# Performance work log

Measured on AMD Instinct MI355X. Metric: run time of the kernel, lower is better.

## Reference

```python
import jax, jax.numpy as jnp
import numpy as np
from jax.scipy.special import gammainc

ALPH = 0.8  # significance level (default arg in original forward)


def _median_width(X, iu, ju):
    # pairwise squared distances; original takes median of strictly-positive
    # strict-upper-triangle entries (tril subtracted) -> median over triu(k=1)
    G = jnp.sum(X * X, axis=1)                    # [n]
    D = G[:, None] + G[None, :] - 2.0 * (X @ X.T)  # [n, n]
    du = D[iu, ju]                                 # strict upper triangle, static size
    return jnp.sqrt(0.5 * jnp.median(du))


def _rbf(X, width):
    G = jnp.sum(X * X, axis=1)
    D = G[:, None] + G[None, :] - 2.0 * (X @ X.T)
    return jnp.exp(-D / (2.0 * width ** 2))


def _center(K):
    # H K H with H = I - 11^T/n  ==  K - rowmean - colmean + totalmean
    cm = jnp.mean(K, axis=0, keepdims=True)   # mean over rows  -> [1, n]
    rm = jnp.mean(K, axis=1, keepdims=True)   # mean over cols  -> [n, 1]
    tm = jnp.mean(K)
    return K - cm - rm + tm


def _gamma_ppf(a, p):
    # invert regularized lower incomplete gamma via fixed-iteration bisection
    hi0 = a + 10.0 * jnp.sqrt(a) + 100.0
    def body(i, lohi):
        lo, hi = lohi
        mid = 0.5 * (lo + hi)
        below = gammainc(a, mid) < p
        return (jnp.where(below, mid, lo), jnp.where(below, hi, mid))
    lo, hi = jax.lax.fori_loop(0, 100, body, (jnp.zeros_like(a), hi0))
    return 0.5 * (lo + hi)


def setup_inputs() -> dict:
    key = jax.random.key(0)
    k1, k2 = jax.random.split(key)
    X = jax.random.normal(k1, (4096, 64), dtype=jnp.float32)
    Y = jax.random.normal(k2, (4096, 64), dtype=jnp.float32)
    return {"X": X, "Y": Y}


def reference(X, Y):
    n = X.shape[0]
    iu, ju = np.triu_indices(n, k=1)  # static index set

    width_x = _median_width(X, iu, ju)
    width_y = _median_width(Y, iu, ju)

    K = _rbf(X, width_x)
    L = _rbf(Y, width_y)

    Kc = _center(K)
    Lc = _center(L)

    testStat = jnp.sum(Kc.T * Lc) / n

    V = (Kc * Lc / 6.0) ** 2
    varHSIC = (jnp.sum(V) - jnp.trace(V)) / n / (n - 1)
    varHSIC = varHSIC * 72.0 * (n - 4) * (n - 5) / n / (n - 1) / (n - 2) / (n - 3)

    # zero-diagonal kernels for mean estimate
    K0sum = jnp.sum(K) - jnp.trace(K)
    L0sum = jnp.sum(L) - jnp.trace(L)
    muX = K0sum / n / (n - 1)
    muY = L0sum / n / (n - 1)
    mHSIC = (1.0 + muX * muY - muX - muY) / n

    al = mHSIC ** 2 / varHSIC
    bet = varHSIC * n / mHSIC
    thresh = bet * _gamma_ppf(al, jnp.float32(1.0 - ALPH))
    return (testStat, thresh)
```

## Files before the change

### kernel.cpp

```cpp
#include <hip/hip_runtime.h>

typedef unsigned int u32;
typedef unsigned short u16;
typedef __attribute__((ext_vector_type(8))) short bf16x8;
typedef __attribute__((ext_vector_type(4))) float f32x4;

#define NPTS 4096
#define DIM  64
#define NB   32
#define NBLK 528
#define WLO16 0x4140u
#define NWBIN 832
#define RSTR 836


__device__ __forceinline__ void bmap(int b, int& by, int& bx){
  by = 0;
  while (b >= NB - by){ b -= NB - by; by++; }
  bx = by + b;
}

__device__ __forceinline__ u16 f2bf(float x){
  u32 u = __float_as_uint(x);
  return (u16)((u + 0x7fffu + ((u>>16)&1u)) >> 16);
}

__global__ __launch_bounds__(256) void convert_k(const float* __restrict__ X, const float* __restrict__ Y,
                                                 u16* __restrict__ Xbf, float* __restrict__ Gall,
                                                 u32* __restrict__ histsum, double* __restrict__ rowK,
                                                 double* __restrict__ rowL, double* __restrict__ sums){
  int t = blockIdx.x*256 + threadIdx.x;
  int rid = t >> 1, hf = t & 1;
  int z = rid >> 12, row = rid & 4095;
  const float* src = (z ? Y : X) + (size_t)row*DIM + hf*32;
  u16* base = Xbf + ((size_t)z*32768 + (size_t)(row>>4)*128 + (row&15))*8;
  float g = 0.f;
#pragma unroll
  for (int f=0; f<4; f++){
    float4 f0 = *(const float4*)(src + f*8);
    float4 f1 = *(const float4*)(src + f*8 + 4);
    g = fmaf(f0.x,f0.x,g); g = fmaf(f0.y,f0.y,g); g = fmaf(f0.z,f0.z,g); g = fmaf(f0.w,f0.w,g);
    g = fmaf(f1.x,f1.x,g); g = fmaf(f1.y,f1.y,g); g = fmaf(f1.z,f1.z,g); g = fmaf(f1.w,f1.w,g);
    ushort4 h0, h1;
    h0.x=f2bf(f0.x); h0.y=f2bf(f0.y); h0.z=f2bf(f0.z); h0.w=f2bf(f0.w);
    h1.x=f2bf(f1.x); h1.y=f2bf(f1.y); h1.z=f2bf(f1.z); h1.w=f2bf(f1.w);
    u16* dst = base + (size_t)(hf*4 + f)*16*8;
    *(ushort4*)dst = h0;
    *(ushort4*)(dst+4) = h1;
  }
  g += __shfl_xor(g, 1, 64);
  if (hf==0) Gall[rid] = g;
  if (t < NPTS){ rowK[t] = 0.0; rowL[t] = 0.0; }
  if (t < 2*RSTR) histsum[t] = 0u;
  if (t < 2) sums[t] = 0.0;
}

__global__ __launch_bounds__(256,2) void hist_k(const u16* __restrict__ Xbf, const float* __restrict__ Gall,
                                                u32* __restrict__ histsum){
  __shared__ u32 lh[RSTR];
  int z = blockIdx.y, tid = threadIdx.x;
  int by,bx; bmap(blockIdx.x, by, bx);
  bool isdiag = (by==bx);
  u32 wgt = isdiag ? 1u : 2u;
  int w=tid>>6, lane=tid&63, q=lane>>4, nl=lane&15;
  for (int t=tid;t<RSTR;t+=256) lh[t]=0;
  __syncthreads();
  const bf16x8* Xb = (const bf16x8*)Xbf + (size_t)z*32768;
  const float* Gz = Gall + z*NPTS;
  int rt0 = w, rt1 = 4 + w;
  int ag0 = by*8 + rt0, ag1 = by*8 + rt1;
  bf16x8 a0f0 = Xb[ag0*128 + q*16 + nl];
  bf16x8 a0f1 = Xb[ag0*128 + (4+q)*16 + nl];
  bf16x8 a1f0 = Xb[ag1*128 + q*16 + nl];
  bf16x8 a1f1 = Xb[ag1*128 + (4+q)*16 + nl];
  float ga0 = Gz[ag0*16 + nl], ga1 = Gz[ag1*16 + nl];
  float g0m[4], g1m[4];
#pragma unroll
  for (int r=0;r<4;r++){ g0m[r] = __shfl(ga0, q*4+r, 64); g1m[r] = __shfl(ga1, q*4+r, 64); }
#pragma unroll
  for (int tb=0;tb<8;tb++){
    int jg = bx*8 + tb;
    bf16x8 bf0 = Xb[jg*128 + q*16 + nl];
    bf16x8 bf1 = Xb[jg*128 + (4+q)*16 + nl];
    f32x4 acc0 = (f32x4)0.0f, acc1 = (f32x4)0.0f;
    acc0 = __builtin_amdgcn_mfma_f32_16x16x32_bf16(a0f0, bf0, acc0, 0,0,0);
    acc0 = __builtin_amdgcn_mfma_f32_16x16x32_bf16(a0f1, bf1, acc0, 0,0,0);
    acc1 = __builtin_amdgcn_mfma_f32_16x16x32_bf16(a1f0, bf0, acc1, 0,0,0);
    acc1 = __builtin_amdgcn_mfma_f32_16x16x32_bf16(a1f1, bf1, acc1, 0,0,0);
    int j = jg*16 + nl;
    float gb = Gz[j];
#pragma unroll
    for (int r=0;r<4;r++){
      float d0 = (g0m[r] + gb) - 2.0f*acc0[r];
      float d1 = (g1m[r] + gb) - 2.0f*acc1[r];
      if (isdiag){
        if (ag0*16 + q*4 + r == j) d0 = 0.f;
        if (ag1*16 + q*4 + r == j) d1 = 0.f;
      }
      u32 t0 = __float_as_uint(d0) >> 16;
      u32 b0 = (t0 < WLO16) ? 0u : (t0 >= WLO16+NWBIN) ? (u32)(NWBIN+1) : (t0 - WLO16 + 1u);
      atomicAdd(&lh[b0], wgt);
      u32 t1 = __float_as_uint(d1) >> 16;
      u32 b1 = (t1 < WLO16) ? 0u : (t1 >= WLO16+NWBIN) ? (u32)(NWBIN+1) : (t1 - WLO16 + 1u);
      atomicAdd(&lh[b1], wgt);
    }
  }
  __syncthreads();
  u32* dst = histsum + (size_t)z*RSTR;
  for (int t=tid;t<RSTR;t+=256){
    u32 v = lh[t];
    if (v) atomicAdd(&dst[t], v);
  }
}

__global__ __launch_bounds__(256) void scan16i(const u32* __restrict__ histsum,
                                               float* __restrict__ scal,
                                               u32 kf1, u32 kf2){
  int z = blockIdx.x;
  int tid = threadIdx.x;
  __shared__ u32 wsum[4];
  __shared__ double svals[2];
  u32 c4[4] = {0,0,0,0};
  if (tid < 209){
    const u32* base = histsum + (size_t)z*RSTR + 4*tid;
    int lim = RSTR - 4*tid;
    c4[0] = base[0];
    if (lim>1) c4[1] = base[1];
    if (lim>2) c4[2] = base[2];
    if (lim>3) c4[3] = base[3];
  }
  u32 s = c4[0]+c4[1]+c4[2]+c4[3];
  int lane = tid & 63, wv = tid >> 6;
  u32 pre = s;
#pragma unroll
  for (int off=1; off<64; off<<=1){
    u32 t2 = __shfl_up(pre, off, 64);
    if (lane >= off) pre += t2;
  }
  if (lane==63) wsum[wv] = pre;
  __syncthreads();
  u32 base2 = 0;
  for (int k=0;k<wv;k++) base2 += wsum[k];
  u32 incl = base2 + pre, excl = incl - s;
  u32 ks[2] = {kf1,kf2};
#pragma unroll
  for (int w2=0; w2<2; w2++){
    if (ks[w2] >= excl && ks[w2] < incl){
      u32 acc = excl;
#pragma unroll
      for (int j=0;j<4;j++){
        if (ks[w2] < acc + c4[j]){
          int b = tid*4 + j;
          double lo, hi;
          if (b==0){ lo=12.0; hi=12.0; }
          else if (b>=NWBIN+1){ lo=1024.0; hi=1024.0; }
          else {
            u32 t16 = WLO16 + (u32)b - 1u;
            lo = (double)__uint_as_float(t16<<16);
            hi = (double)__uint_as_float((t16+1u)<<16);
          }
          double frac = ((double)(ks[w2]-acc) + 0.5)/(double)c4[j];
          svals[w2] = lo + (hi-lo)*frac;
          break;
        }
        acc += c4[j];
      }
    }
  }
  __syncthreads();
  if (tid==0){
    float med = (float)(0.5*(svals[0]+svals[1]));
    float wd = sqrtf(0.5f*med);
    scal[z] = 2.0f*wd*wd;
  }
}

__global__ __launch_bounds__(256,2) void rowsum_k(const u16* __restrict__ Xbf, const float* __restrict__ Gall,
                                                  const float* __restrict__ scal,
                                                  double* __restrict__ rowK, double* __restrict__ rowL,
                                                  double* __restrict__ sums){
  __shared__ double rowacc[128];
  __shared__ double colLDS[4][128];
  __shared__ double tred[2];
  int z = blockIdx.y, tid = threadIdx.x;
  int by,bx; bmap(blockIdx.x, by, bx);
  bool isdiag = (by==bx);
  int w=tid>>6, lane=tid&63, q=lane>>4, nl=lane&15;
  const bf16x8* Xb = (const bf16x8*)Xbf + (size_t)z*32768;
  const float* Gz = Gall + z*NPTS;
  float negi = -1.0f/scal[z];
  int rt0 = w, rt1 = 4 + w;
  int ag0 = by*8 + rt0, ag1 = by*8 + rt1;
  bf16x8 a0f0 = Xb[ag0*128 + q*16 + nl];
  bf16x8 a0f1 = Xb[ag0*128 + (4+q)*16 + nl];
  bf16x8 a1f0 = Xb[ag1*128 + q*16 + nl];
  bf16x8 a1f1 = Xb[ag1*128 + (4+q)*16 + nl];
  float ga0 = Gz[ag0*16 + nl], ga1 = Gz[ag1*16 + nl];
  float g0m[4], g1m[4];
#pragma unroll
  for (int r=0;r<4;r++){ g0m[r] = __shfl(ga0, q*4+r, 64); g1m[r] = __shfl(ga1, q*4+r, 64); }
  double rs0[4] = {0,0,0,0}, rs1[4] = {0,0,0,0};
#pragma unroll
  for (int tb=0;tb<8;tb++){
    int jg = bx*8 + tb;
    bf16x8 bf0 = Xb[jg*128 + q*16 + nl];
    bf16x8 bf1 = Xb[jg*128 + (4+q)*16 + nl];
    f32x4 acc0 = (f32x4)0.0f, acc1 = (f32x4)0.0f;
    acc0 = __builtin_amdgcn_mfma_f32_16x16x32_bf16(a0f0, bf0, acc0, 0,0,0);
    acc0 = __builtin_amdgcn_mfma_f32_16x16x32_bf16(a0f1, bf1, acc0, 0,0,0);
    acc1 = __builtin_amdgcn_mfma_f32_16x16x32_bf16(a1f0, bf0, acc1, 0,0,0);
    acc1 = __builtin_amdgcn_mfma_f32_16x16x32_bf16(a1f1, bf1, acc1, 0,0,0);
    int j = jg*16 + nl;
    float gb = Gz[j];
    double cs = 0.0;
#pragma unroll
    for (int r=0;r<4;r++){
      float d0 = (g0m[r] + gb) - 2.0f*acc0[r];
      float d1 = (g1m[r] + gb) - 2.0f*acc1[r];
      if (isdiag){
        if (ag0*16 + q*4 + r == j) d0 = 0.f;
        if (ag1*16 + q*4 + r == j) d1 = 0.f;
      }
      double e0 = (double)expf(d0*negi);
      double e1 = (double)expf(d1*negi);
      rs0[r] += e0; rs1[r] += e1;
      cs += e0 + e1;
    }
    cs += __shfl_xor(cs, 16, 64);
    cs += __shfl_xor(cs, 32, 64);
    if (q==0) colLDS[w][tb*16 + nl] = cs;
  }
#pragma unroll
  for (int r=0;r<4;r++){
    double v0 = rs0[r], v1 = rs1[r];
    v0 += __shfl_xor(v0,1,64); v0 += __shfl_xor(v0,2,64);
    v0 += __shfl_xor(v0,4,64); v0 += __shfl_xor(v0,8,64);
    v1 += __shfl_xor(v1,1,64); v1 += __shfl_xor(v1,2,64);
    v1 += __shfl_xor(v1,4,64); v1 += __shfl_xor(v1,8,64);
    rs0[r] = v0; rs1[r] = v1;
  }
  if (nl==0){
#pragma unroll
    for (int r=0;r<4;r++){
      rowacc[rt0*16 + q*4 + r] = rs0[r];
      rowacc[rt1*16 + q*4 + r] = rs1[r];
    }
  }
  __syncthreads();
  double tot = 0.0;
  if (tid < 128){
    double rv = rowacc[tid];
    double cv = colLDS[0][tid] + colLDS[1][tid] + colLDS[2][tid] + colLDS[3][tid];
    double* rowG = z ? rowL : rowK;
    atomicAdd(&rowG[by*128 + tid], rv);
    if (!isdiag) atomicAdd(&rowG[bx*128 + tid], cv);
    tot = rv + (isdiag ? 0.0 : cv);
  }
#pragma unroll
  for (int s2=1;s2<64;s2<<=1) tot += __shfl_xor(tot, s2, 64);
  if (lane==0 && w<2) tred[w] = tot;
  __syncthreads();
  if (tid==0) atomicAdd(&sums[z], tred[0] + tred[1]);
}

__global__ __launch_bounds__(256,2) void final_k(const u16* __restrict__ Xbf, const float* __restrict__ Gall,
                                                 const float* __restrict__ scal,
                                                 const double* __restrict__ rowK,
                                                 const double* __restrict__ rowL,
                                                 const double* __restrict__ sums,
                                                 double* __restrict__ partials){
  int tid = threadIdx.x;
  int b = blockIdx.x >> 1, half = blockIdx.x & 1;
  int by,bx; bmap(b,by,bx);
  bool isdiag = (by==bx);
  int w=tid>>6, lane=tid&63, q=lane>>4, nl=lane&15;
  const bf16x8* Xb = (const bf16x8*)Xbf;
  const bf16x8* Yb = Xb + 32768;
  const float* Gx = Gall;
  const float* Gy = Gall + NPTS;
  const double inv_n = 1.0/(double)NPTS;
  double tmK = sums[0]*(inv_n*inv_n), tmL = sums[1]*(inv_n*inv_n);
  float negx = -1.0f/scal[0], negy = -1.0f/scal[1];
  double wgt = isdiag ? 1.0 : 2.0;
  double S1=0, S2=0, trV=0;
  int rt = half*4 + w;
  int ag = by*8 + rt;
  bf16x8 axf0 = Xb[ag*128 + q*16 + nl];
  bf16x8 axf1 = Xb[ag*128 + (4+q)*16 + nl];
  bf16x8 ayf0 = Yb[ag*128 + q*16 + nl];
  bf16x8 ayf1 = Yb[ag*128 + (4+q)*16 + nl];
  int rowA = ag*16 + nl;
  float gaX = Gx[rowA], gaY = Gy[rowA];
  float gXm[4], gYm[4];
#pragma unroll
  for (int r=0;r<4;r++){ gXm[r] = __shfl(gaX, q*4+r, 64); gYm[r] = __shfl(gaY, q*4+r, 64); }
  double rmKi[4], rmLi[4];
#pragma unroll
  for (int r=0;r<4;r++){
    int i = ag*16 + q*4 + r;
    rmKi[r] = rowK[i]*inv_n; rmLi[r] = rowL[i]*inv_n;
  }
#pragma unroll
  for (int tb=0;tb<8;tb++){
    int jg = bx*8 + tb;
    f32x4 accX = (f32x4)0.0f, accY = (f32x4)0.0f;
    accX = __builtin_amdgcn_mfma_f32_16x16x32_bf16(axf0, Xb[jg*128 + q*16 + nl],     accX, 0,0,0);
    accX = __builtin_amdgcn_mfma_f32_16x16x32_bf16(axf1, Xb[jg*128 + (4+q)*16 + nl], accX, 0,0,0);
    accY = __builtin_amdgcn_mfma_f32_16x16x32_bf16(ayf0, Yb[jg*128 + q*16 + nl],     accY, 0,0,0);
    accY = __builtin_amdgcn_mfma_f32_16x16x32_bf16(ayf1, Yb[jg*128 + (4+q)*16 + nl], accY, 0,0,0);
    int j = jg*16 + nl;
    float gbX = Gx[j], gbY = Gy[j];
    double cmK = rowK[j]*inv_n - tmK;
    double cmL = rowL[j]*inv_n - tmL;
#pragma unroll
    for (int r=0;r<4;r++){
      int i = ag*16 + q*4 + r;
      float dx = (gXm[r] + gbX) - 2.0f*accX[r];
      float dy = (gYm[r] + gbY) - 2.0f*accY[r];
      bool dg = isdiag && i==j;
      if (dg){ dx = 0.f; dy = 0.f; }
      float kx = expf(dx*negx);
      float lv = expf(dy*negy);
      double kc = ((double)kx - rmKi[r]) - cmK;
      double lc = ((double)lv - rmLi[r]) - cmL;
      double prod = kc*lc;
      S1 += wgt*prod;
      double vv = (prod*prod)*(1.0/36.0);
      S2 += wgt*vv;
      if (dg) trV += vv;
    }
  }
  __shared__ double red[4][3];
  double vals[3]={S1,S2,trV};
  int wv = tid >> 6;
#pragma unroll
  for (int v=0;v<3;v++){
    double x = vals[v];
#pragma unroll
    for (int s2=1;s2<64;s2<<=1) x += __shfl_xor(x, s2, 64);
    if (lane==0) red[wv][v]=x;
  }
  __syncthreads();
  if (tid < 3)
    partials[(size_t)blockIdx.x*4 + tid] = red[0][tid]+red[1][tid]+red[2][tid]+red[3][tid];
}

__device__ double gammainc_wave(double a, double x, double lga, int lane){
  double C = 1.0/a;
  double psum = 0.0;
  for (int b=0;b<8192;b++){
    double k = (double)(b*64 + lane + 1);
    double rr = x/(a+k);
    double pp = rr;
#pragma unroll
    for (int s=1;s<64;s<<=1){
      double t = __shfl_up(pp, s, 64);
      if (lane >= s) pp *= t;
    }
    double c = C*pp;
    psum += c;
    double clast = __shfl(c, 63, 64);
    double rlast = __shfl(rr, 63, 64);
    C = clast;
    if (rlast < 1.0 && clast*rlast/(1.0-rlast) < 1e-17) break;
  }
#pragma unroll
  for (int s=1;s<64;s<<=1) psum += __shfl_xor(psum, s, 64);
  double total = 1.0/a + psum;
  return exp(-x + a*log(x) - lga) * total;
}

__global__ __launch_bounds__(256) void finalize_k(const double* __restrict__ partials,
                                                  const double* __restrict__ sums,
                                                  float* __restrict__ out)
{
  __shared__ double red[3][4];
  __shared__ double tot[4];
  int tid = threadIdx.x;
  double v0=0,v1=0,v2=0;
  for (int i=tid; i<2*NBLK; i+=256){
    const double* p = partials + (size_t)i*4;
    v0+=p[0]; v1+=p[1]; v2+=p[2];
  }
  double vals[3]={v0,v1,v2};
  int lane = tid & 63, wv = tid >> 6;
#pragma unroll
  for (int v=0;v<3;v++){
    double x = vals[v];
#pragma unroll
    for (int s2=1;s2<64;s2<<=1) x += __shfl_xor(x, s2, 64);
    if (lane==0) red[v][wv]=x;
  }
  __syncthreads();
  if (tid==0){
#pragma unroll
    for (int v=0;v<3;v++) tot[v] = red[v][0]+red[v][1]+red[v][2]+red[v][3];
  }
  __syncthreads();
  if (tid >= 64) return;

  const double n = (double)NPTS;
  double totK=sums[0], totL=sums[1];
  double S1=tot[0], S2=tot[1], trV=tot[2];
  double testStat = S1/n;
  double varHSIC = (S2 - trV)/n/(n-1.0);
  varHSIC = varHSIC*72.0*(n-4.0)*(n-5.0)/n/(n-1.0)/(n-2.0)/(n-3.0);
  double muX = (totK-n)/n/(n-1.0);
  double muY = (totL-n)/n/(n-1.0);
  double mHSIC = (1.0 + muX*muY - muX - muY)/n;
  double al = mHSIC*mHSIC/varHSIC;
  double bet = varHSIC*n/mHSIC;
  double p = (double)((float)(1.0-0.8));
  double lga = lgamma(al);
  double lo = 0.0, hi = al + 10.0*sqrt(al) + 100.0;
  const double zp = -0.8416212335729142957;
  double t = 1.0 - 1.0/(9.0*al) + zp/(3.0*sqrt(al));
  double x = al*t*t*t;
  if (!(x > 0.0) || !(x < hi)) x = 0.5*hi;
  for (int it=0; it<2; ++it){
    double P = gammainc_wave(al, x, lga, lane);
    double diff = P - p;
    if (diff < 0.0) lo = x; else hi = x;
    if (fabs(diff) < 1e-12) break;
    double pdf = exp(-x + (al-1.0)*log(x) - lga);
    double nx = x - diff/pdf;
    if (!(nx > lo) || !(nx < hi)) nx = 0.5*(lo+hi);
    x = nx;
  }
  if (lane==0){
    out[0]=(float)testStat;
    out[1]=(float)(bet*x);
  }
}

extern "C" void kernel_launch(void* const* d_in, const int* in_sizes, int n_in,
                              void* d_out, int out_size, void* d_ws, size_t ws_size,
                              hipStream_t stream) {
  const float* X = (const float*)d_in[0];
  const float* Y = (const float*)d_in[1];
  float* out = (float*)d_out;
  char* ws = (char*)d_ws;

  double* sums     = (double*)ws;
  float*  scal     = (float*)(ws + 128);
  u32*    histsum  = (u32*)(ws + 256);
  double* rowK     = (double*)(ws + 8192);
  double* rowL     = (double*)(ws + 40960);
  float*  Gall     = (float*)(ws + 73728);
  double* partials = (double*)(ws + 106496);
  u16*    Xbf      = (u16*)(ws + (4u<<20));
  size_t need = (size_t)(4u<<20) + (size_t)2*NPTS*DIM*2;

  if (ws_size < need) return;

  const u32 KF1 = 4096u + 2u*4193279u;
  const u32 KF2 = 4096u + 2u*4193280u;

  convert_k<<<64,256,0,stream>>>(X, Y, Xbf, Gall, histsum, rowK, rowL, sums);
  hist_k<<<dim3(NBLK,2),256,0,stream>>>(Xbf, Gall, histsum);
  scan16i<<<2,256,0,stream>>>(histsum, scal, KF1, KF2);
  rowsum_k<<<dim3(NBLK,2),256,0,stream>>>(Xbf, Gall, scal, rowK, rowL, sums);
  final_k<<<2*NBLK,256,0,stream>>>(Xbf, Gall, scal, rowK, rowL, sums, partials);
  finalize_k<<<1,256,0,stream>>>(partials, sums, out);
}
```

Baseline: 146.9 us.

## Fuse median scan into rowsum, last-block finalize, and privatize histograms

Every rowsum block now redundantly runs the histogram prefix scan to find the median width, so the separate scan kernel launch goes away. The final reduction and gamma-quantile solve move into final_k, where a global atomic counter elects the last block to do them, removing the finalize kernel launch. The per-block LDS histogram is split into four lane-indexed copies to cut atomic contention, and global double sums are spread over slots to reduce same-address atomics. In exchange, every rowsum block repeats the scan work, and the last final_k block carries the serial gamma computation.

Result: slower. 153.6 us (+4.6%).

```diff
diff --git a/kernel.cpp b/kernel.cpp
--- a/kernel.cpp
+++ b/kernel.cpp
@@ -12,6 +12,8 @@
 #define WLO16 0x4140u
 #define NWBIN 832
 #define RSTR 836
+#define KF1C 8390654u
+#define KF2C 8390656u
 
 
 __device__ __forceinline__ void bmap(int b, int& by, int& bx){
@@ -28,12 +30,13 @@
 __global__ __launch_bounds__(256) void convert_k(const float* __restrict__ X, const float* __restrict__ Y,
                                                  u16* __restrict__ Xbf, float* __restrict__ Gall,
                                                  u32* __restrict__ histsum, double* __restrict__ rowK,
-                                                 double* __restrict__ rowL, double* __restrict__ sums){
+                                                 double* __restrict__ rowL, double* __restrict__ sumsS,
+                                                 double* __restrict__ slotbuf, u32* __restrict__ ctr){
   int t = blockIdx.x*256 + threadIdx.x;
   int rid = t >> 1, hf = t & 1;
   int z = rid >> 12, row = rid & 4095;
   const float* src = (z ? Y : X) + (size_t)row*DIM + hf*32;
-  u16* base = Xbf + ((size_t)z*32768 + (size_t)(row>>4)*128 + (row&15))*8;
+  u16* basep = Xbf + ((size_t)z*32768 + (size_t)(row>>4)*128 + (row&15))*8;
   float g = 0.f;
 #pragma unroll
   for (int f=0; f<4; f++){
@@ -44,7 +47,7 @@
     ushort4 h0, h1;
     h0.x=f2bf(f0.x); h0.y=f2bf(f0.y); h0.z=f2bf(f0.z); h0.w=f2bf(f0.w);
     h1.x=f2bf(f1.x); h1.y=f2bf(f1.y); h1.z=f2bf(f1.z); h1.w=f2bf(f1.w);
-    u16* dst = base + (size_t)(hf*4 + f)*16*8;
+    u16* dst = basep + (size_t)(hf*4 + f)*16*8;
     *(ushort4*)dst = h0;
     *(ushort4*)(dst+4) = h1;
   }
@@ -52,23 +55,25 @@
   if (hf==0) Gall[rid] = g;
   if (t < NPTS){ rowK[t] = 0.0; rowL[t] = 0.0; }
   if (t < 2*RSTR) histsum[t] = 0u;
-  if (t < 2) sums[t] = 0.0;
+  if (t < 64) slotbuf[t] = 0.0;
+  if (t < 16) sumsS[t] = 0.0;
+  if (t == 0) *ctr = 0u;
 }
 
 __global__ __launch_bounds__(256,2) void hist_k(const u16* __restrict__ Xbf, const float* __restrict__ Gall,
                                                 u32* __restrict__ histsum){
-  __shared__ u32 lh[RSTR];
+  __shared__ u32 lh[4][RSTR];
   int z = blockIdx.y, tid = threadIdx.x;
   int by,bx; bmap(blockIdx.x, by, bx);
   bool isdiag = (by==bx);
   u32 wgt = isdiag ? 1u : 2u;
   int w=tid>>6, lane=tid&63, q=lane>>4, nl=lane&15;
-  for (int t=tid;t<RSTR;t+=256) lh[t]=0;
+  int cp = lane & 3;
+  for (int t=tid;t<4*RSTR;t+=256) ((u32*)lh)[t]=0;
   __syncthreads();
   const bf16x8* Xb = (const bf16x8*)Xbf + (size_t)z*32768;
   const float* Gz = Gall + z*NPTS;
-  int rt0 = w, rt1 = 4 + w;
-  int ag0 = by*8 + rt0, ag1 = by*8 + rt1;
+  int ag0 = by*8 + w, ag1 = by*8 + 4 + w;
   bf16x8 a0f0 = Xb[ag0*128 + q*16 + nl];
   bf16x8 a0f1 = Xb[ag0*128 + (4+q)*16 + nl];
   bf16x8 a1f0 = Xb[ag1*128 + q*16 + nl];
@@ -98,99 +103,97 @@
         if (ag1*16 + q*4 + r == j) d1 = 0.f;
       }
       u32 t0 = __float_as_uint(d0) >> 16;
-      u32 b0 = (t0 < WLO16) ? 0u : (t0 >= WLO16+NWBIN) ? (u32)(NWBIN+1) : (t0 - WLO16 + 1u);
-      atomicAdd(&lh[b0], wgt);
+      u32 bin0 = (t0 < WLO16) ? 0u : (t0 >= WLO16+NWBIN) ? (u32)(NWBIN+1) : (t0 - WLO16 + 1u);
+      atomicAdd(&lh[cp][bin0], wgt);
       u32 t1 = __float_as_uint(d1) >> 16;
-      u32 b1 = (t1 < WLO16) ? 0u : (t1 >= WLO16+NWBIN) ? (u32)(NWBIN+1) : (t1 - WLO16 + 1u);
-      atomicAdd(&lh[b1], wgt);
+      u32 bin1 = (t1 < WLO16) ? 0u : (t1 >= WLO16+NWBIN) ? (u32)(NWBIN+1) : (t1 - WLO16 + 1u);
+      atomicAdd(&lh[cp][bin1], wgt);
     }
   }
   __syncthreads();
   u32* dst = histsum + (size_t)z*RSTR;
   for (int t=tid;t<RSTR;t+=256){
-    u32 v = lh[t];
+    u32 v = lh[0][t] + lh[1][t] + lh[2][t] + lh[3][t];
     if (v) atomicAdd(&dst[t], v);
   }
 }
 
-__global__ __launch_bounds__(256) void scan16i(const u32* __restrict__ histsum,
-                                               float* __restrict__ scal,
-                                               u32 kf1, u32 kf2){
-  int z = blockIdx.x;
-  int tid = threadIdx.x;
-  __shared__ u32 wsum[4];
-  __shared__ double svals[2];
-  u32 c4[4] = {0,0,0,0};
-  if (tid < 209){
-    const u32* base = histsum + (size_t)z*RSTR + 4*tid;
-    int lim = RSTR - 4*tid;
-    c4[0] = base[0];
-    if (lim>1) c4[1] = base[1];
-    if (lim>2) c4[2] = base[2];
-    if (lim>3) c4[3] = base[3];
-  }
-  u32 s = c4[0]+c4[1]+c4[2]+c4[3];
-  int lane = tid & 63, wv = tid >> 6;
-  u32 pre = s;
-#pragma unroll
-  for (int off=1; off<64; off<<=1){
-    u32 t2 = __shfl_up(pre, off, 64);
-    if (lane >= off) pre += t2;
-  }
-  if (lane==63) wsum[wv] = pre;
-  __syncthreads();
-  u32 base2 = 0;
-  for (int k=0;k<wv;k++) base2 += wsum[k];
-  u32 incl = base2 + pre, excl = incl - s;
-  u32 ks[2] = {kf1,kf2};
-#pragma unroll
-  for (int w2=0; w2<2; w2++){
-    if (ks[w2] >= excl && ks[w2] < incl){
-      u32 acc = excl;
-#pragma unroll
-      for (int j=0;j<4;j++){
-        if (ks[w2] < acc + c4[j]){
-          int b = tid*4 + j;
-          double lo, hi;
-          if (b==0){ lo=12.0; hi=12.0; }
-          else if (b>=NWBIN+1){ lo=1024.0; hi=1024.0; }
-          else {
-            u32 t16 = WLO16 + (u32)b - 1u;
-            lo = (double)__uint_as_float(t16<<16);
-            hi = (double)__uint_as_float((t16+1u)<<16);
+__global__ __launch_bounds__(256,2) void rowsum_k(const u16* __restrict__ Xbf, const float* __restrict__ Gall,
+                                                  const u32* __restrict__ histsum, float* __restrict__ scal,
+                                                  double* __restrict__ rowK, double* __restrict__ rowL,
+                                                  double* __restrict__ sumsS){
+  __shared__ union {
+    struct { u32 wsum[4]; double svals[2]; float scal_sh; } sc;
+    struct { double rowacc[128]; double colLDS[4][128]; double tred[2]; } rs;
+  } sh;
+  int z = blockIdx.y, tid = threadIdx.x;
+  int w=tid>>6, lane=tid&63, q=lane>>4, nl=lane&15;
+
+  {
+    u32 c4[4] = {0,0,0,0};
+    if (tid < 209){
+      const u32* base = histsum + (size_t)z*RSTR + 4*tid;
+      int lim = RSTR - 4*tid;
+      c4[0] = base[0];
+      if (lim>1) c4[1] = base[1];
+      if (lim>2) c4[2] = base[2];
+      if (lim>3) c4[3] = base[3];
+    }
+    u32 s = c4[0]+c4[1]+c4[2]+c4[3];
+    u32 pre = s;
+#pragma unroll
+    for (int off=1; off<64; off<<=1){
+      u32 t2 = __shfl_up(pre, off, 64);
+      if (lane >= off) pre += t2;
+    }
+    if (lane==63) sh.sc.wsum[w] = pre;
+    __syncthreads();
+    u32 base2 = 0;
+    for (int k=0;k<w;k++) base2 += sh.sc.wsum[k];
+    u32 incl = base2 + pre, excl = incl - s;
+    u32 ks[2] = {KF1C,KF2C};
+#pragma unroll
+    for (int w2=0; w2<2; w2++){
+      if (ks[w2] >= excl && ks[w2] < incl){
+        u32 acc = excl;
+#pragma unroll
+        for (int j=0;j<4;j++){
+          if (ks[w2] < acc + c4[j]){
+            int b = tid*4 + j;
+            double lo, hi;
+            if (b==0){ lo=12.0; hi=12.0; }
+            else if (b>=NWBIN+1){ lo=1024.0; hi=1024.0; }
+            else {
+              u32 t16 = WLO16 + (u32)b - 1u;
+              lo = (double)__uint_as_float(t16<<16);
+              hi = (double)__uint_as_float((t16+1u)<<16);
+            }
+            double frac = ((double)(ks[w2]-acc) + 0.5)/(double)c4[j];
+            sh.sc.svals[w2] = lo + (hi-lo)*frac;
+            break;
           }
-          double frac = ((double)(ks[w2]-acc) + 0.5)/(double)c4[j];
-          svals[w2] = lo + (hi-lo)*frac;
-          break;
+          acc += c4[j];
         }
-        acc += c4[j];
       }
     }
-  }
-  __syncthreads();
-  if (tid==0){
-    float med = (float)(0.5*(svals[0]+svals[1]));
-    float wd = sqrtf(0.5f*med);
-    scal[z] = 2.0f*wd*wd;
-  }
-}
-
-__global__ __launch_bounds__(256,2) void rowsum_k(const u16* __restrict__ Xbf, const float* __restrict__ Gall,
-                                                  const float* __restrict__ scal,
-                                                  double* __restrict__ rowK, double* __restrict__ rowL,
-                                                  double* __restrict__ sums){
-  __shared__ double rowacc[128];
-  __shared__ double colLDS[4][128];
-  __shared__ double tred[2];
-  int z = blockIdx.y, tid = threadIdx.x;
+    __syncthreads();
+    if (tid==0){
+      float med = (float)(0.5*(sh.sc.svals[0]+sh.sc.svals[1]));
+      float wd = sqrtf(0.5f*med);
+      float sc2 = 2.0f*wd*wd;
+      sh.sc.scal_sh = sc2;
+      if (blockIdx.x==0) scal[z] = sc2;
+    }
+    __syncthreads();
+  }
+  float negi = -1.0f / sh.sc.scal_sh;
+  __syncthreads();
+
   int by,bx; bmap(blockIdx.x, by, bx);
   bool isdiag = (by==bx);
-  int w=tid>>6, lane=tid&63, q=lane>>4, nl=lane&15;
   const bf16x8* Xb = (const bf16x8*)Xbf + (size_t)z*32768;
   const float* Gz = Gall + z*NPTS;
-  float negi = -1.0f/scal[z];
-  int rt0 = w, rt1 = 4 + w;
-  int ag0 = by*8 + rt0, ag1 = by*8 + rt1;
+  int ag0 = by*8 + w, ag1 = by*8 + 4 + w;
   bf16x8 a0f0 = Xb[ag0*128 + q*16 + nl];
   bf16x8 a0f1 = Xb[ag0*128 + (4+q)*16 + nl];
   bf16x8 a1f0 = Xb[ag1*128 + q*16 + nl];
@@ -228,7 +231,7 @@
     }
     cs += __shfl_xor(cs, 16, 64);
     cs += __shfl_xor(cs, 32, 64);
-    if (q==0) colLDS[w][tb*16 + nl] = cs;
+    if (q==0) sh.rs.colLDS[w][tb*16 + nl] = cs;
   }
 #pragma unroll
   for (int r=0;r<4;r++){
@@ -242,15 +245,15 @@
   if (nl==0){
 #pragma unroll
     for (int r=0;r<4;r++){
-      rowacc[rt0*16 + q*4 + r] = rs0[r];
-      rowacc[rt1*16 + q*4 + r] = rs1[r];
+      sh.rs.rowacc[w*16 + q*4 + r]     = rs0[r];
+      sh.rs.rowacc[(4+w)*16 + q*4 + r] = rs1[r];
     }
   }
   __syncthreads();
   double tot = 0.0;
   if (tid < 128){
-    double rv = rowacc[tid];
-    double cv = colLDS[0][tid] + colLDS[1][tid] + colLDS[2][tid] + colLDS[3][tid];
+    double rv = sh.rs.rowacc[tid];
+    double cv = sh.rs.colLDS[0][tid] + sh.rs.colLDS[1][tid] + sh.rs.colLDS[2][tid] + sh.rs.colLDS[3][tid];
     double* rowG = z ? rowL : rowK;
     atomicAdd(&rowG[by*128 + tid], rv);
     if (!isdiag) atomicAdd(&rowG[bx*128 + tid], cv);
@@ -258,17 +261,45 @@
   }
 #pragma unroll
   for (int s2=1;s2<64;s2<<=1) tot += __shfl_xor(tot, s2, 64);
-  if (lane==0 && w<2) tred[w] = tot;
-  __syncthreads();
-  if (tid==0) atomicAdd(&sums[z], tred[0] + tred[1]);
+  if (lane==0 && w<2) sh.rs.tred[w] = tot;
+  __syncthreads();
+  if (tid==0) atomicAdd(&sumsS[z*8 + (blockIdx.x & 7)], sh.rs.tred[0] + sh.rs.tred[1]);
+}
+
+__device__ double gammainc_wave(double a, double x, double lga, int lane){
+  double C = 1.0/a;
+  double psum = 0.0;
+  for (int b=0;b<8192;b++){
+    double k = (double)(b*64 + lane + 1);
+    double rr = x/(a+k);
+    double pp = rr;
+#pragma unroll
+    for (int s=1;s<64;s<<=1){
+      double t = __shfl_up(pp, s, 64);
+      if (lane >= s) pp *= t;
+    }
+    double c = C*pp;
+    psum += c;
+    double clast = __shfl(c, 63, 64);
+    double rlast = __shfl(rr, 63, 64);
+    C = clast;
+    if (rlast < 1.0 && clast*rlast/(1.0-rlast) < 1e-17) break;
+  }
+#pragma unroll
+  for (int s=1;s<64;s<<=1) psum += __shfl_xor(psum, s, 64);
+  double total = 1.0/a + psum;
+  return exp(-x + a*log(x) - lga) * total;
 }
 
 __global__ __launch_bounds__(256,2) void final_k(const u16* __restrict__ Xbf, const float* __restrict__ Gall,
                                                  const float* __restrict__ scal,
                                                  const double* __restrict__ rowK,
                                                  const double* __restrict__ rowL,
-                                                 const double* __restrict__ sums,
-                                                 double* __restrict__ partials){
+                                                 const double* __restrict__ sumsS,
+                                                 double* __restrict__ slotbuf, u32* __restrict__ ctr,
+                                                 float* __restrict__ out){
+  __shared__ double red[4][3];
+  __shared__ int lastFlag;
   int tid = threadIdx.x;
   int b = blockIdx.x >> 1, half = blockIdx.x & 1;
   int by,bx; bmap(b,by,bx);
@@ -279,12 +310,14 @@
   const float* Gx = Gall;
   const float* Gy = Gall + NPTS;
   const double inv_n = 1.0/(double)NPTS;
-  double tmK = sums[0]*(inv_n*inv_n), tmL = sums[1]*(inv_n*inv_n);
+  double sK=0.0, sL=0.0;
+#pragma unroll
+  for (int k2=0;k2<8;k2++){ sK += sumsS[k2]; sL += sumsS[8+k2]; }
+  double tmK = sK*(inv_n*inv_n), tmL = sL*(inv_n*inv_n);
   float negx = -1.0f/scal[0], negy = -1.0f/scal[1];
   double wgt = isdiag ? 1.0 : 2.0;
   double S1=0, S2=0, trV=0;
-  int rt = half*4 + w;
-  int ag = by*8 + rt;
+  int ag = by*8 + half*4 + w;
   bf16x8 axf0 = Xb[ag*128 + q*16 + nl];
   bf16x8 axf1 = Xb[ag*128 + (4+q)*16 + nl];
   bf16x8 ayf0 = Yb[ag*128 + q*16 + nl];
@@ -330,83 +363,49 @@
       if (dg) trV += vv;
     }
   }
-  __shared__ double red[4][3];
   double vals[3]={S1,S2,trV};
-  int wv = tid >> 6;
 #pragma unroll
   for (int v=0;v<3;v++){
     double x = vals[v];
 #pragma unroll
     for (int s2=1;s2<64;s2<<=1) x += __shfl_xor(x, s2, 64);
-    if (lane==0) red[wv][v]=x;
-  }
-  __syncthreads();
-  if (tid < 3)
-    partials[(size_t)blockIdx.x*4 + tid] = red[0][tid]+red[1][tid]+red[2][tid]+red[3][tid];
-}
-
-__device__ double gammainc_wave(double a, double x, double lga, int lane){
-  double C = 1.0/a;
-  double psum = 0.0;
-  for (int b=0;b<8192;b++){
-    double k = (double)(b*64 + lane + 1);
-    double rr = x/(a+k);
-    double pp = rr;
-#pragma unroll
-    for (int s=1;s<64;s<<=1){
-      double t = __shfl_up(pp, s, 64);
-      if (lane >= s) pp *= t;
-    }
-    double c = C*pp;
-    psum += c;
-    double clast = __shfl(c, 63, 64);
-    double rlast = __shfl(rr, 63, 64);
-    C = clast;
-    if (rlast < 1.0 && clast*rlast/(1.0-rlast) < 1e-17) break;
-  }
-#pragma unroll
-  for (int s=1;s<64;s<<=1) psum += __shfl_xor(psum, s, 64);
-  double total = 1.0/a + psum;
-  return exp(-x + a*log(x) - lga) * total;
-}
-
-__global__ __launch_bounds__(256) void finalize_k(const double* __restrict__ partials,
-                                                  const double* __restrict__ sums,
-                                                  float* __restrict__ out)
-{
-  __shared__ double red[3][4];
-  __shared__ double tot[4];
-  int tid = threadIdx.x;
-  double v0=0,v1=0,v2=0;
-  for (int i=tid; i<2*NBLK; i+=256){
-    const double* p = partials + (size_t)i*4;
-    v0+=p[0]; v1+=p[1]; v2+=p[2];
-  }
-  double vals[3]={v0,v1,v2};
-  int lane = tid & 63, wv = tid >> 6;
-#pragma unroll
-  for (int v=0;v<3;v++){
-    double x = vals[v];
-#pragma unroll
-    for (int s2=1;s2<64;s2<<=1) x += __shfl_xor(x, s2, 64);
-    if (lane==0) red[v][wv]=x;
+    if (lane==0) red[w][v]=x;
+  }
+  __syncthreads();
+  if (tid < 3){
+    double val = red[0][tid]+red[1][tid]+red[2][tid]+red[3][tid];
+    atomicAdd(&slotbuf[(size_t)(blockIdx.x & 15)*4 + tid], val);
   }
   __syncthreads();
   if (tid==0){
-#pragma unroll
-    for (int v=0;v<3;v++) tot[v] = red[v][0]+red[v][1]+red[v][2]+red[v][3];
-  }
-  __syncthreads();
+    __threadfence();
+    u32 old = atomicAdd(ctr, 1u);
+    lastFlag = (old == (u32)(2*NBLK - 1)) ? 1 : 0;
+  }
+  __syncthreads();
+  if (!lastFlag) return;
+
   if (tid >= 64) return;
-
+  double t0=0.0, t1=0.0, t2=0.0;
+  if (lane < 16){
+    double* sp = slotbuf + (size_t)lane*4;
+    t0 = atomicAdd(&sp[0], 0.0);
+    t1 = atomicAdd(&sp[1], 0.0);
+    t2 = atomicAdd(&sp[2], 0.0);
+  }
+#pragma unroll
+  for (int s2=1;s2<64;s2<<=1){
+    t0 += __shfl_xor(t0, s2, 64);
+    t1 += __shfl_xor(t1, s2, 64);
+    t2 += __shfl_xor(t2, s2, 64);
+  }
   const double n = (double)NPTS;
-  double totK=sums[0], totL=sums[1];
-  double S1=tot[0], S2=tot[1], trV=tot[2];
-  double testStat = S1/n;
-  double varHSIC = (S2 - trV)/n/(n-1.0);
+  double S1t=t0, S2t=t1, trVt=t2;
+  double testStat = S1t/n;
+  double varHSIC = (S2t - trVt)/n/(n-1.0);
   varHSIC = varHSIC*72.0*(n-4.0)*(n-5.0)/n/(n-1.0)/(n-2.0)/(n-3.0);
-  double muX = (totK-n)/n/(n-1.0);
-  double muY = (totL-n)/n/(n-1.0);
+  double muX = (sK-n)/n/(n-1.0);
+  double muY = (sL-n)/n/(n-1.0);
   double mHSIC = (1.0 + muX*muY - muX - muY)/n;
   double al = mHSIC*mHSIC/varHSIC;
   double bet = varHSIC*n/mHSIC;
@@ -414,8 +413,8 @@
   double lga = lgamma(al);
   double lo = 0.0, hi = al + 10.0*sqrt(al) + 100.0;
   const double zp = -0.8416212335729142957;
-  double t = 1.0 - 1.0/(9.0*al) + zp/(3.0*sqrt(al));
-  double x = al*t*t*t;
+  double tt = 1.0 - 1.0/(9.0*al) + zp/(3.0*sqrt(al));
+  double x = al*tt*tt*tt;
   if (!(x > 0.0) || !(x < hi)) x = 0.5*hi;
   for (int it=0; it<2; ++it){
     double P = gammainc_wave(al, x, lga, lane);
@@ -441,25 +440,21 @@
   float* out = (float*)d_out;
   char* ws = (char*)d_ws;
 
-  double* sums     = (double*)ws;
+  double* sumsS    = (double*)ws;
   float*  scal     = (float*)(ws + 128);
   u32*    histsum  = (u32*)(ws + 256);
+  double* slotbuf  = (double*)(ws + 7168);
+  u32*    ctr      = (u32*)(ws + 7680);
   double* rowK     = (double*)(ws + 8192);
   double* rowL     = (double*)(ws + 40960);
   float*  Gall     = (float*)(ws + 73728);
-  double* partials = (double*)(ws + 106496);
   u16*    Xbf      = (u16*)(ws + (4u<<20));
   size_t need = (size_t)(4u<<20) + (size_t)2*NPTS*DIM*2;
 
   if (ws_size < need) return;
 
-  const u32 KF1 = 4096u + 2u*4193279u;
-  const u32 KF2 = 4096u + 2u*4193280u;
-
-  convert_k<<<64,256,0,stream>>>(X, Y, Xbf, Gall, histsum, rowK, rowL, sums);
+  convert_k<<<64,256,0,stream>>>(X, Y, Xbf, Gall, histsum, rowK, rowL, sumsS, slotbuf, ctr);
   hist_k<<<dim3(NBLK,2),256,0,stream>>>(Xbf, Gall, histsum);
-  scan16i<<<2,256,0,stream>>>(histsum, scal, KF1, KF2);
-  rowsum_k<<<dim3(NBLK,2),256,0,stream>>>(Xbf, Gall, scal, rowK, rowL, sums);
-  final_k<<<2*NBLK,256,0,stream>>>(Xbf, Gall, scal, rowK, rowL, sums, partials);
-  finalize_k<<<1,256,0,stream>>>(partials, sums, out);
-}
+  rowsum_k<<<dim3(NBLK,2),256,0,stream>>>(Xbf, Gall, histsum, scal, rowK, rowL, sumsS);
+  final_k<<<2*NBLK,256,0,stream>>>(Xbf, Gall, scal, rowK, rowL, sumsS, slotbuf, ctr, out);
+}
```
